# Optimization experiments

Measured on AMD Instinct MI355X. Metric: run time of the kernel, lower is better.

Reference implementation:

```python
import jax, jax.numpy as jnp
import numpy as np

C_IMG = 16
GRID = 128
NV = 100000
NE = 1600000
CH = (32, 64, 64)
SCALE = 0.1
STEPS = 1
SLOPE = 0.3  # LeakyReLU default in module


def setup_inputs() -> dict:
    key = jax.random.key(0)
    ks = jax.random.split(key, 20)
    image_features = jax.random.normal(ks[0], (C_IMG, GRID, GRID, GRID), jnp.float32)
    # vertices live in voxel coordinates of the feature grid
    vertices = jax.random.uniform(ks[1], (NV, 3), jnp.float32) * (GRID - 1)
    edge_src = jax.random.randint(ks[2], (NE,), 0, NV, jnp.int32)
    edge_dst = jax.random.randint(ks[3], (NE,), 0, NV, jnp.int32)
    dims = [C_IMG + 3] + list(CH) + [3]  # +3 normalized positions
    inp = {"image_features": image_features, "vertices": vertices,
           "edge_src": edge_src, "edge_dst": edge_dst}
    ki = 4
    for i in range(len(dims) - 1):
        fan_in = dims[i]
        s = 1.0 / np.sqrt(fan_in)
        inp[f"w_self{i}"] = jax.random.normal(ks[ki], (dims[i], dims[i + 1]), jnp.float32) * s
        inp[f"w_nb{i}"] = jax.random.normal(ks[ki + 1], (dims[i], dims[i + 1]), jnp.float32) * s
        inp[f"b{i}"] = jnp.zeros((dims[i + 1],), jnp.float32)
        ki += 2
    return inp


def trilinear_sample(img, verts):
    # img: (C, W, H, D); verts: (V, 3) voxel coords -> (V, C)
    C, W, H, D = img.shape
    hi = jnp.array([W - 1, H - 1, D - 1], verts.dtype)
    p = jnp.clip(verts, 0.0, hi)
    p0 = jnp.floor(p)
    i0 = p0.astype(jnp.int32)
    i1 = jnp.minimum(i0 + 1, hi.astype(jnp.int32))
    w = p - p0
    x0, y0, z0 = i0[:, 0], i0[:, 1], i0[:, 2]
    x1, y1, z1 = i1[:, 0], i1[:, 1], i1[:, 2]
    wx, wy, wz = w[:, 0:1], w[:, 1:2], w[:, 2:3]

    def g(xi, yi, zi):
        return img[:, xi, yi, zi].T  # (V, C)

    c00 = g(x0, y0, z0) * (1 - wz) + g(x0, y0, z1) * wz
    c01 = g(x0, y1, z0) * (1 - wz) + g(x0, y1, z1) * wz
    c10 = g(x1, y0, z0) * (1 - wz) + g(x1, y0, z1) * wz
    c11 = g(x1, y1, z0) * (1 - wz) + g(x1, y1, z1) * wz
    return (c00 * (1 - wy) + c01 * wy) * (1 - wx) + (c10 * (1 - wy) + c11 * wy) * wx


def edge_conv(x, src, dst, inv_deg, w_self, w_nb, b):
    nb = jax.ops.segment_sum(x[src], dst, num_segments=x.shape[0]) * inv_deg
    return x @ w_self + nb @ w_nb + b


def reference(image_features, vertices, edge_src, edge_dst,
              w_self0, w_nb0, b0, w_self1, w_nb1, b1,
              w_self2, w_nb2, b2, w_self3, w_nb3, b3):
    nv = vertices.shape[0]
    deg = jax.ops.segment_sum(jnp.ones((edge_src.shape[0],), jnp.float32), edge_dst,
                              num_segments=nv)
    inv_deg = (1.0 / jnp.maximum(deg, 1.0))[:, None]
    grid_max = jnp.float32(max(image_features.shape[1:]))  # image_shape.max()
    layers = [(w_self0, w_nb0, b0), (w_self1, w_nb1, b1), (w_self2, w_nb2, b2)]
    for _ in range(STEPS):
        feats = trilinear_sample(image_features, vertices)
        feats = jnp.concatenate([vertices / grid_max, feats], axis=-1)
        h = feats
        for (ws, wn, b) in layers:
            h = jax.nn.leaky_relu(edge_conv(h, edge_src, edge_dst, inv_deg, ws, wn, b), SLOPE)
        deformation = edge_conv(h, edge_src, edge_dst, inv_deg, w_self3, w_nb3, b3)
        vertices = vertices + SCALE * deformation
    return vertices
```

## Files before the change

kernel.cpp:

```cpp
#include <hip/hip_runtime.h>

#define C_IMG 16
#define GRIDSZ 128
#define VOL (GRIDSZ * GRIDSZ * GRIDSZ)
#define SLOPE 0.3f
#define SCALE 0.1f
#define EPB 4096
#define HEPB 16384
#define BIN_CAP 16384

using f4_t  = __attribute__((ext_vector_type(4))) float;
using bf8_t = __attribute__((ext_vector_type(8))) short;

__device__ __forceinline__ unsigned int bf16_pack2(float a, float b) {
    unsigned int ua = __float_as_uint(a);
    ua = (ua + 0x7FFFu + ((ua >> 16) & 1u)) >> 16;
    unsigned int ub = __float_as_uint(b);
    ub = (ub + 0x7FFFu + ((ub >> 16) & 1u)) >> 16;
    return ua | (ub << 16);
}
__device__ __forceinline__ unsigned short bf16_1(float a) {
    unsigned int ua = __float_as_uint(a);
    return (unsigned short)((ua + 0x7FFFu + ((ua >> 16) & 1u)) >> 16);
}
__device__ __forceinline__ float bf_lo(unsigned int u) { return __uint_as_float(u << 16); }
__device__ __forceinline__ float bf_hi(unsigned int u) { return __uint_as_float(u & 0xFFFF0000u); }

__global__ __launch_bounds__(256) void k_hist(const int* __restrict__ edst,
                                              int* __restrict__ bucketCount, int ne) {
    __shared__ int h[256];
    const int tid = threadIdx.x;
    h[tid] = 0;
    __syncthreads();
    const int base = blockIdx.x * HEPB;
    const int n = min(HEPB, ne - base);
    for (int i = tid; i < n; i += 256)
        atomicAdd(&h[((unsigned)edst[base + i]) >> 9], 1);
    __syncthreads();
    if (h[tid]) atomicAdd(&bucketCount[tid], h[tid]);
}

__global__ __launch_bounds__(256) void k_scan256(const int* __restrict__ bucketCount,
                                                 int* __restrict__ bucketBase,
                                                 int* __restrict__ bucketCursor,
                                                 int* __restrict__ rowStart,
                                                 int np, int nv, int ne) {
    __shared__ int buf[256];
    const int tid = threadIdx.x;
    const int v = (tid < np) ? bucketCount[tid] : 0;
    buf[tid] = v;
    __syncthreads();
    #pragma unroll
    for (int off = 1; off < 256; off <<= 1) {
        int t = (tid >= off) ? buf[tid - off] : 0;
        __syncthreads();
        buf[tid] += t;
        __syncthreads();
    }
    const int excl = buf[tid] - v;
    bucketBase[tid] = excl;
    bucketCursor[tid] = excl;
    if (tid == 0) {
        bucketBase[np] = ne;
        rowStart[nv] = ne;
    }
}

__global__ __launch_bounds__(256) void k_bucket(const int* __restrict__ esrc,
                                                const int* __restrict__ edst,
                                                int* __restrict__ bucketCursor,
                                                unsigned int* __restrict__ pairs, int ne) {
    __shared__ unsigned int hist[256];
    __shared__ unsigned int pref[256];
    __shared__ unsigned int curs[256];
    __shared__ unsigned int gbase[256];
    __shared__ unsigned int stage_v[EPB];
    __shared__ unsigned char stage_b[EPB];
    const int tid = threadIdx.x;
    const int base = blockIdx.x * EPB;
    const int n = min(EPB, ne - base);
    hist[tid] = 0;
    __syncthreads();
    for (int i = tid; i < n; i += 256)
        atomicAdd(&hist[((unsigned)edst[base + i]) >> 9], 1u);
    __syncthreads();
    const unsigned int h = hist[tid];
    pref[tid] = h;
    __syncthreads();
    #pragma unroll
    for (int off = 1; off < 256; off <<= 1) {
        unsigned int t = (tid >= off) ? pref[tid - off] : 0;
        __syncthreads();
        pref[tid] += t;
        __syncthreads();
    }
    const unsigned int excl = pref[tid] - h;
    gbase[tid] = h ? (unsigned int)atomicAdd(&bucketCursor[tid], (int)h) : 0u;
    __syncthreads();
    pref[tid] = excl;
    curs[tid] = excl;
    __syncthreads();
    for (int i = tid; i < n; i += 256) {
        unsigned int d = (unsigned)edst[base + i];
        unsigned int s = (unsigned)esrc[base + i];
        unsigned int p = atomicAdd(&curs[d >> 9], 1u);
        stage_v[p] = (s << 9) | (d & 511u);
        stage_b[p] = (unsigned char)(d >> 9);
    }
    __syncthreads();
    for (int i = tid; i < n; i += 256) {
        unsigned int b = stage_b[i];
        pairs[gbase[b] + (unsigned)i - pref[b]] = stage_v[i];
    }
}

__global__ __launch_bounds__(256) void k_binsort(const unsigned int* __restrict__ pairs,
                                                 const int* __restrict__ bucketBase,
                                                 int* __restrict__ rowStart,
                                                 float* __restrict__ invdeg,
                                                 int* __restrict__ csrSrc, int nv) {
    __shared__ int deg_s[512];
    __shared__ int rs_s[512];
    __shared__ int cur_s[512];
    __shared__ int scan_s[256];
    __shared__ int outbuf[BIN_CAP];
    const int tid = threadIdx.x;
    const int b = blockIdx.x;
    const int vbase = b << 9;
    if (vbase >= nv) return;
    const int nvb = min(512, nv - vbase);
    const int gs = bucketBase[b];
    const int ge = bucketBase[b + 1];
    const int count = ge - gs;
    deg_s[tid] = 0;
    deg_s[tid + 256] = 0;
    __syncthreads();
    for (int i = tid; i < count; i += 256) {
        unsigned int p = pairs[gs + i];
        atomicAdd(&deg_s[p & 511u], 1);
    }
    __syncthreads();
    const int d0 = deg_s[2 * tid];
    const int d1 = deg_s[2 * tid + 1];
    const int ps = d0 + d1;
    scan_s[tid] = ps;
    __syncthreads();
    #pragma unroll
    for (int off = 1; off < 256; off <<= 1) {
        int t = (tid >= off) ? scan_s[tid - off] : 0;
        __syncthreads();
        scan_s[tid] += t;
        __syncthreads();
    }
    const int epair = scan_s[tid] - ps;
    rs_s[2 * tid] = epair;
    rs_s[2 * tid + 1] = epair + d0;
    cur_s[2 * tid] = epair;
    cur_s[2 * tid + 1] = epair + d0;
    #pragma unroll
    for (int u = 0; u < 2; ++u) {
        int idx = 2 * tid + u;
        if (idx < nvb) {
            rowStart[vbase + idx] = gs + rs_s[idx];
            int d = deg_s[idx];
            invdeg[vbase + idx] = 1.0f / (float)(d > 1 ? d : 1);
        }
    }
    __syncthreads();
    if (count <= BIN_CAP) {
        for (int i = tid; i < count; i += 256) {
            unsigned int p = pairs[gs + i];
            int pos = atomicAdd(&cur_s[p & 511u], 1);
            outbuf[pos] = (int)(p >> 9);
        }
        __syncthreads();
        for (int i = tid; i < count; i += 256) csrSrc[gs + i] = outbuf[i];
    } else {
        for (int i = tid; i < count; i += 256) {
            unsigned int p = pairs[gs + i];
            int pos = atomicAdd(&cur_s[p & 511u], 1);
            csrSrc[gs + pos] = (int)(p >> 9);
        }
    }
}

__global__ __launch_bounds__(256) void k_transpose(const float* __restrict__ img,
                                                   unsigned int* __restrict__ timg) {
    const int t = blockIdx.x * 256 + threadIdx.x;
    const int q  = t & 3;
    const int z4 = (t >> 2) & 31;
    const int xy = t >> 7;
    const int z0 = z4 * 4;
    const int c0 = q * 4;
    const size_t base = (size_t)xy * GRIDSZ + z0;
    float4 v0 = *(const float4*)(img + (size_t)(c0 + 0) * VOL + base);
    float4 v1 = *(const float4*)(img + (size_t)(c0 + 1) * VOL + base);
    float4 v2 = *(const float4*)(img + (size_t)(c0 + 2) * VOL + base);
    float4 v3 = *(const float4*)(img + (size_t)(c0 + 3) * VOL + base);
    #pragma unroll
    for (int j = 0; j < 4; ++j) {
        float f0 = (j == 0) ? v0.x : (j == 1) ? v0.y : (j == 2) ? v0.z : v0.w;
        float f1 = (j == 0) ? v1.x : (j == 1) ? v1.y : (j == 2) ? v1.z : v1.w;
        float f2 = (j == 0) ? v2.x : (j == 1) ? v2.y : (j == 2) ? v2.z : v2.w;
        float f3 = (j == 0) ? v3.x : (j == 1) ? v3.y : (j == 2) ? v3.z : v3.w;
        uint2 o;
        o.x = bf16_pack2(f0, f1);
        o.y = bf16_pack2(f2, f3);
        *(uint2*)(timg + (size_t)(xy * GRIDSZ + z0 + j) * 8 + q * 2) = o;
    }
}

__global__ __launch_bounds__(256) void k_sample(const unsigned int* __restrict__ timg,
                                                const float* __restrict__ verts,
                                                unsigned int* __restrict__ feats, int nv) {
    int t = blockIdx.x * 256 + threadIdx.x;
    int v = t >> 1;
    int q = t & 1;
    if (v >= nv) return;
    float px = verts[v * 3 + 0];
    float py = verts[v * 3 + 1];
    float pz = verts[v * 3 + 2];
    float cx = fminf(fmaxf(px, 0.0f), 127.0f);
    float cy = fminf(fmaxf(py, 0.0f), 127.0f);
    float cz = fminf(fmaxf(pz, 0.0f), 127.0f);
    float fx = floorf(cx), fy = floorf(cy), fz = floorf(cz);
    int x0 = (int)fx, y0 = (int)fy, z0 = (int)fz;
    int x1 = min(x0 + 1, 127), y1 = min(y0 + 1, 127), z1 = min(z0 + 1, 127);
    float wx = cx - fx, wy = cy - fy, wz = cz - fz;
    const int qo = q * 4;
    #define LD(X, Y, Z) (*(const uint4*)(timg + ((size_t)((((X) << 7) + (Y)) << 7) + (size_t)(Z)) * 8 + qo))
    uint4 f000 = LD(x0, y0, z0), f001 = LD(x0, y0, z1);
    uint4 f010 = LD(x0, y1, z0), f011 = LD(x0, y1, z1);
    uint4 f100 = LD(x1, y0, z0), f101 = LD(x1, y0, z1);
    uint4 f110 = LD(x1, y1, z0), f111 = LD(x1, y1, z1);
    #undef LD
    float r[8];
    const unsigned int* a000 = (const unsigned int*)&f000;
    const unsigned int* a001 = (const unsigned int*)&f001;
    const unsigned int* a010 = (const unsigned int*)&f010;
    const unsigned int* a011 = (const unsigned int*)&f011;
    const unsigned int* a100 = (const unsigned int*)&f100;
    const unsigned int* a101 = (const unsigned int*)&f101;
    const unsigned int* a110 = (const unsigned int*)&f110;
    const unsigned int* a111 = (const unsigned int*)&f111;
    #pragma unroll
    for (int u = 0; u < 4; ++u) {
        float c00l = bf_lo(a000[u]) * (1.f - wz) + bf_lo(a001[u]) * wz;
        float c01l = bf_lo(a010[u]) * (1.f - wz) + bf_lo(a011[u]) * wz;
        float c10l = bf_lo(a100[u]) * (1.f - wz) + bf_lo(a101[u]) * wz;
        float c11l = bf_lo(a110[u]) * (1.f - wz) + bf_lo(a111[u]) * wz;
        r[2 * u] = (c00l * (1.f - wy) + c01l * wy) * (1.f - wx) +
                   (c10l * (1.f - wy) + c11l * wy) * wx;
        float c00h = bf_hi(a000[u]) * (1.f - wz) + bf_hi(a001[u]) * wz;
        float c01h = bf_hi(a010[u]) * (1.f - wz) + bf_hi(a011[u]) * wz;
        float c10h = bf_hi(a100[u]) * (1.f - wz) + bf_hi(a101[u]) * wz;
        float c11h = bf_hi(a110[u]) * (1.f - wz) + bf_hi(a111[u]) * wz;
        r[2 * u + 1] = (c00h * (1.f - wy) + c01h * wy) * (1.f - wx) +
                       (c10h * (1.f - wy) + c11h * wy) * wx;
    }
    unsigned int* row = feats + (size_t)v * 16;
    uint4 o;
    o.x = bf16_pack2(r[0], r[1]); o.y = bf16_pack2(r[2], r[3]);
    o.z = bf16_pack2(r[4], r[5]); o.w = bf16_pack2(r[6], r[7]);
    *(uint4*)(row + q * 4) = o;
    if (q == 0) {
        uint4 o2;
        o2.x = bf16_pack2(px * (1.0f / 128.0f), py * (1.0f / 128.0f));
        o2.y = bf16_pack2(pz * (1.0f / 128.0f), 0.0f);
        o2.z = 0u; o2.w = 0u;
        *(uint4*)(row + 8) = o2;
        *(uint4*)(row + 12) = make_uint4(0u, 0u, 0u, 0u);
    }
}

template <int SU>
__global__ __launch_bounds__(256) void k_gather16(const unsigned int* __restrict__ x,
                                                  const int* __restrict__ rowStart,
                                                  const int* __restrict__ csrSrc,
                                                  const float* __restrict__ invdeg,
                                                  unsigned int* __restrict__ nb, int nv) {
    constexpr int NCH = SU / 4;
    int t = blockIdx.x * 256 + threadIdx.x;
    int v = t / NCH;
    if (v >= nv) return;
    int ch = t - v * NCH;
    int beg = rowStart[v];
    int end = rowStart[v + 1];
    float a0 = 0.f, a1 = 0.f, a2 = 0.f, a3 = 0.f, a4 = 0.f, a5 = 0.f, a6 = 0.f, a7 = 0.f;
    int j = beg;
    for (; j + 3 < end; j += 4) {
        int s0 = csrSrc[j];
        int s1 = csrSrc[j + 1];
        int s2 = csrSrc[j + 2];
        int s3 = csrSrc[j + 3];
        uint4 q0 = ((const uint4*)(x + (size_t)s0 * SU))[ch];
        uint4 q1 = ((const uint4*)(x + (size_t)s1 * SU))[ch];
        uint4 q2 = ((const uint4*)(x + (size_t)s2 * SU))[ch];
        uint4 q3 = ((const uint4*)(x + (size_t)s3 * SU))[ch];
        a0 += bf_lo(q0.x); a1 += bf_hi(q0.x);
        a2 += bf_lo(q0.y); a3 += bf_hi(q0.y);
        a4 += bf_lo(q0.z); a5 += bf_hi(q0.z);
        a6 += bf_lo(q0.w); a7 += bf_hi(q0.w);
        a0 += bf_lo(q1.x); a1 += bf_hi(q1.x);
        a2 += bf_lo(q1.y); a3 += bf_hi(q1.y);
        a4 += bf_lo(q1.z); a5 += bf_hi(q1.z);
        a6 += bf_lo(q1.w); a7 += bf_hi(q1.w);
        a0 += bf_lo(q2.x); a1 += bf_hi(q2.x);
        a2 += bf_lo(q2.y); a3 += bf_hi(q2.y);
        a4 += bf_lo(q2.z); a5 += bf_hi(q2.z);
        a6 += bf_lo(q2.w); a7 += bf_hi(q2.w);
        a0 += bf_lo(q3.x); a1 += bf_hi(q3.x);
        a2 += bf_lo(q3.y); a3 += bf_hi(q3.y);
        a4 += bf_lo(q3.z); a5 += bf_hi(q3.z);
        a6 += bf_lo(q3.w); a7 += bf_hi(q3.w);
    }
    for (; j < end; ++j) {
        int s = csrSrc[j];
        uint4 q = ((const uint4*)(x + (size_t)s * SU))[ch];
        a0 += bf_lo(q.x); a1 += bf_hi(q.x);
        a2 += bf_lo(q.y); a3 += bf_hi(q.y);
        a4 += bf_lo(q.z); a5 += bf_hi(q.z);
        a6 += bf_lo(q.w); a7 += bf_hi(q.w);
    }
    const float id = invdeg[v];
    uint4 o;
    o.x = bf16_pack2(a0 * id, a1 * id); o.y = bf16_pack2(a2 * id, a3 * id);
    o.z = bf16_pack2(a4 * id, a5 * id); o.w = bf16_pack2(a6 * id, a7 * id);
    ((uint4*)(nb + (size_t)v * SU))[ch] = o;
}

template <int KX, int COUT, bool REMAP0, int VALID_CIN, bool PREMUL>
__global__ __launch_bounds__(256) void k_layer_mfma(const unsigned int* __restrict__ x,
                                                    const unsigned int* __restrict__ nbs,
                                                    const float* __restrict__ Ws,
                                                    const float* __restrict__ Wn,
                                                    const float* __restrict__ bias,
                                                    unsigned int* __restrict__ out, int nv,
                                                    const float* __restrict__ Wn3,
                                                    unsigned int* __restrict__ zout) {
    constexpr int KTOT = 2 * KX;
    constexpr int KW = KTOT + 8;
    constexpr int NT = COUT / 16;
    constexpr int MT = 2;
    constexpr int SXU = KX / 2;
    constexpr int KS = KX / 32;
    __shared__ __align__(16) unsigned short bt[COUT * KW];
    __shared__ float wn3_s[192];

    for (int i = threadIdx.x; i < COUT * KTOT; i += 256) {
        int c = i / KTOT;
        int kk = i - c * KTOT;
        int j = (kk < KX) ? kk : kk - KX;
        const float* W = (kk < KX) ? Ws : Wn;
        float w = 0.f;
        if (j < VALID_CIN) {
            int sr = REMAP0 ? ((j < 16) ? (j + 3) : (j - 16)) : j;
            w = W[sr * COUT + c];
        }
        bt[c * KW + kk] = bf16_1(w);
    }
    if constexpr (PREMUL) {
        if (threadIdx.x < 192) wn3_s[threadIdx.x] = Wn3[threadIdx.x];
    }
    __syncthreads();

    const int lane = threadIdx.x & 63;
    const int wid = threadIdx.x >> 6;
    const int v0 = blockIdx.x * (4 * MT * 16) + wid * (MT * 16);
    const int row = lane & 15;
    const int kg = lane >> 4;

    f4_t acc[MT][NT] = {};

    #pragma unroll
    for (int ks = 0; ks < 2 * KS; ++ks) {
        const unsigned int* src = (ks < KS) ? x : nbs;
        const int kbase = (ks < KS) ? ks * 32 : (ks - KS) * 32;
        bf8_t afrag[MT];
        #pragma unroll
        for (int mt = 0; mt < MT; ++mt) {
            int v = v0 + mt * 16 + row;
            v = min(v, nv - 1);
            afrag[mt] = *(const bf8_t*)(src + (size_t)v * SXU + ((kbase + kg * 8) >> 1));
        }
        #pragma unroll
        for (int nt = 0; nt < NT; ++nt) {
            bf8_t bfrag = *(const bf8_t*)(bt + (nt * 16 + row) * KW + ks * 32 + kg * 8);
            #pragma unroll
            for (int mt = 0; mt < MT; ++mt)
                acc[mt][nt] = __builtin_amdgcn_mfma_f32_16x16x32_bf16(afrag[mt], bfrag,
                                                                      acc[mt][nt], 0, 0, 0);
        }
    }

    unsigned short* po = (unsigned short*)out;
    float bq[NT];
    #pragma unroll
    for (int nt = 0; nt < NT; ++nt) bq[nt] = bias[nt * 16 + row];
    #pragma unroll
    for (int mt = 0; mt < MT; ++mt) {
        #pragma unroll
        for (int r = 0; r < 4; ++r) {
            const int v = v0 + mt * 16 + kg * 4 + r;
            float tv[NT];
            #pragma unroll
            for (int nt = 0; nt < NT; ++nt) {
                float t = acc[mt][nt][r] + bq[nt];
                t = (t >= 0.f) ? t : SLOPE * t;
                tv[nt] = t;
                if (v < nv) po[(size_t)v * COUT + nt * 16 + row] = bf16_1(t);
            }
            if constexpr (PREMUL) {
                float z0 = 0.f, z1 = 0.f, z2 = 0.f;
                #pragma unroll
                for (int nt = 0; nt < NT; ++nt) {
                    const float* wr = wn3_s + (nt * 16 + row) * 3;
                    z0 += tv[nt] * wr[0];
                    z1 += tv[nt] * wr[1];
                    z2 += tv[nt] * wr[2];
                }
                #pragma unroll
                for (int m = 1; m < 16; m <<= 1) {
                    z0 += __shfl_xor(z0, m);
                    z1 += __shfl_xor(z1, m);
                    z2 += __shfl_xor(z2, m);
                }
                if (row == 0 && v < nv) {
                    uint2 o;
                    o.x = bf16_pack2(z0, z1);
                    o.y = bf16_pack2(z2, 0.f);
                    *(uint2*)(zout + (size_t)v * 2) = o;
                }
            }
        }
    }
}

__global__ __launch_bounds__(256) void k_final(const unsigned int* __restrict__ h,
                                               const unsigned int* __restrict__ z,
                                               const int* __restrict__ rowStart,
                                               const int* __restrict__ csrSrc,
                                               const float* __restrict__ invdeg,
                                               const float* __restrict__ ws,
                                               const float* __restrict__ b,
                                               const float* __restrict__ verts,
                                               float* __restrict__ out, int nv) {
    __shared__ float w_s[64 * 3];
    if (threadIdx.x < 64 * 3) w_s[threadIdx.x] = ws[threadIdx.x];
    __syncthreads();
    int v = blockIdx.x * 256 + threadIdx.x;
    if (v >= nv) return;
    float n0 = 0.f, n1 = 0.f, n2 = 0.f;
    {
        int beg = rowStart[v];
        int end = rowStart[v + 1];
        int j = beg;
        for (; j + 3 < end; j += 4) {
            int s0 = csrSrc[j];
            int s1 = csrSrc[j + 1];
            int s2 = csrSrc[j + 2];
            int s3 = csrSrc[j + 3];
            uint2 q0 = *(const uint2*)(z + (size_t)s0 * 2);
            uint2 q1 = *(const uint2*)(z + (size_t)s1 * 2);
            uint2 q2 = *(const uint2*)(z + (size_t)s2 * 2);
            uint2 q3 = *(const uint2*)(z + (size_t)s3 * 2);
            n0 += bf_lo(q0.x); n1 += bf_hi(q0.x); n2 += bf_lo(q0.y);
            n0 += bf_lo(q1.x); n1 += bf_hi(q1.x); n2 += bf_lo(q1.y);
            n0 += bf_lo(q2.x); n1 += bf_hi(q2.x); n2 += bf_lo(q2.y);
            n0 += bf_lo(q3.x); n1 += bf_hi(q3.x); n2 += bf_lo(q3.y);
        }
        for (; j < end; ++j) {
            int s = csrSrc[j];
            uint2 q = *(const uint2*)(z + (size_t)s * 2);
            n0 += bf_lo(q.x); n1 += bf_hi(q.x); n2 += bf_lo(q.y);
        }
    }
    const uint4* hr = (const uint4*)(h + (size_t)v * 32);
    float a0 = b[0], a1 = b[1], a2 = b[2];
    #pragma unroll
    for (int q = 0; q < 8; ++q) {
        uint4 hv = hr[q];
        float f[8] = {bf_lo(hv.x), bf_hi(hv.x), bf_lo(hv.y), bf_hi(hv.y),
                      bf_lo(hv.z), bf_hi(hv.z), bf_lo(hv.w), bf_hi(hv.w)};
        #pragma unroll
        for (int i = 0; i < 8; ++i) {
            int k = q * 8 + i;
            a0 += f[i] * w_s[k * 3 + 0];
            a1 += f[i] * w_s[k * 3 + 1];
            a2 += f[i] * w_s[k * 3 + 2];
        }
    }
    float id = invdeg[v];
    a0 += n0 * id; a1 += n1 * id; a2 += n2 * id;
    out[(size_t)v * 3 + 0] = verts[(size_t)v * 3 + 0] + SCALE * a0;
    out[(size_t)v * 3 + 1] = verts[(size_t)v * 3 + 1] + SCALE * a1;
    out[(size_t)v * 3 + 2] = verts[(size_t)v * 3 + 2] + SCALE * a2;
}

extern "C" void kernel_launch(void* const* d_in, const int* in_sizes, int n_in,
                              void* d_out, int out_size, void* d_ws, size_t ws_size,
                              hipStream_t stream) {
    const float* img   = (const float*)d_in[0];
    const float* verts = (const float*)d_in[1];
    const int*   esrc  = (const int*)d_in[2];
    const int*   edst  = (const int*)d_in[3];
    const float* ws0 = (const float*)d_in[4];
    const float* wn0 = (const float*)d_in[5];
    const float* b0  = (const float*)d_in[6];
    const float* ws1 = (const float*)d_in[7];
    const float* wn1 = (const float*)d_in[8];
    const float* b1  = (const float*)d_in[9];
    const float* ws2 = (const float*)d_in[10];
    const float* wn2 = (const float*)d_in[11];
    const float* b2  = (const float*)d_in[12];
    const float* ws3 = (const float*)d_in[13];
    const float* wn3 = (const float*)d_in[14];
    const float* b3  = (const float*)d_in[15];

    const int nv = in_sizes[1] / 3;
    const int ne = in_sizes[2];

    char* base = (char*)d_ws;
    size_t off = 0;
    auto alloc = [&](size_t bytes) -> void* {
        off = (off + 255) & ~(size_t)255;
        void* p = base + off;
        off += bytes;
        return p;
    };
    float* invdeg   = (float*)alloc((size_t)nv * 4);
    int*   rowStart = (int*)alloc((size_t)(nv + 1) * 4);
    int*   bucketCount  = (int*)alloc(256 * 4);
    int*   bucketBase   = (int*)alloc(257 * 4);
    int*   bucketCursor = (int*)alloc(256 * 4);
    int*   csrSrc   = (int*)alloc((size_t)ne * 4);
    unsigned int* A   = (unsigned int*)alloc((size_t)nv * 32 * 4);
    unsigned int* B   = (unsigned int*)alloc((size_t)nv * 32 * 4);
    unsigned int* NBu = (unsigned int*)alloc((size_t)nv * 32 * 4);
    unsigned int* Z   = (unsigned int*)alloc((size_t)nv * 2 * 4);
    unsigned int* timg = (unsigned int*)alloc((size_t)VOL * 16 * 2);
    unsigned int* pairs = (unsigned int*)NBu;

    auto blocks = [](long long n) { return (int)((n + 255) / 256); };
    const int nbuckets = (nv + 511) >> 9;
    const int lb = (nv + 127) / 128;

    k_transpose<<<(GRIDSZ * GRIDSZ * 32 * 4) / 256, 256, 0, stream>>>(img, timg);

    hipMemsetAsync(bucketCount, 0, 256 * 4, stream);
    k_hist<<<(ne + HEPB - 1) / HEPB, 256, 0, stream>>>(edst, bucketCount, ne);
    k_scan256<<<1, 256, 0, stream>>>(bucketCount, bucketBase, bucketCursor, rowStart, nbuckets, nv, ne);
    k_bucket<<<(ne + EPB - 1) / EPB, 256, 0, stream>>>(esrc, edst, bucketCursor, pairs, ne);
    k_binsort<<<nbuckets, 256, 0, stream>>>(pairs, bucketBase, rowStart, invdeg, csrSrc, nv);

    k_sample<<<blocks((long long)nv * 2), 256, 0, stream>>>(timg, verts, A, nv);

    k_gather16<16><<<blocks((long long)nv * 4), 256, 0, stream>>>(A, rowStart, csrSrc, invdeg, NBu, nv);
    k_layer_mfma<32, 32, true, 19, false><<<lb, 256, 0, stream>>>(
        A, NBu, ws0, wn0, b0, B, nv, nullptr, nullptr);

    k_gather16<16><<<blocks((long long)nv * 4), 256, 0, stream>>>(B, rowStart, csrSrc, invdeg, NBu, nv);
    k_layer_mfma<32, 64, false, 32, false><<<lb, 256, 0, stream>>>(
        B, NBu, ws1, wn1, b1, A, nv, nullptr, nullptr);

    k_gather16<32><<<blocks((long long)nv * 8), 256, 0, stream>>>(A, rowStart, csrSrc, invdeg, NBu, nv);
    k_layer_mfma<64, 64, false, 64, true><<<lb, 256, 0, stream>>>(
        A, NBu, ws2, wn2, b2, B, nv, wn3, Z);

    k_final<<<blocks(nv), 256, 0, stream>>>(
        B, Z, rowStart, csrSrc, invdeg, ws3, b3, verts, (float*)d_out, nv);
}
```

Before: 459.6 us.

## Fuse neighbor gather into MFMA layer kernels and merge preprocessing launches

Each layer's neighbor aggregation now runs inside the MFMA layer kernel, writing the averaged neighbor features into shared memory instead of a global NB buffer. This removes the global write and re-read of the NB buffer and three kernel launches. The image transpose and edge histogram are merged into one launch, and the separate scan kernel is removed: k_bucket and k_binsort each recompute the bucket prefix redundantly per block. The cost is lower gather parallelism per vertex block, since 256 threads share 128 vertices with a serialized loop. Shared memory use per block also rises, which may reduce occupancy.

After: 454.3 us. Within noise of the previous version (-1.1%).

```diff
diff --git a/kernel.cpp b/kernel.cpp
--- a/kernel.cpp
+++ b/kernel.cpp
@@ -7,6 +7,7 @@
 #define SCALE 0.1f
 #define EPB 4096
 #define HEPB 16384
+#define TBLOCKS 8192
 #define BIN_CAP 16384
 
 using f4_t  = __attribute__((ext_vector_type(4))) float;
@@ -26,61 +27,77 @@
 __device__ __forceinline__ float bf_lo(unsigned int u) { return __uint_as_float(u << 16); }
 __device__ __forceinline__ float bf_hi(unsigned int u) { return __uint_as_float(u & 0xFFFF0000u); }
 
-__global__ __launch_bounds__(256) void k_hist(const int* __restrict__ edst,
-                                              int* __restrict__ bucketCount, int ne) {
+__global__ __launch_bounds__(256) void k_pre(const float* __restrict__ img,
+                                             unsigned int* __restrict__ timg,
+                                             const int* __restrict__ edst,
+                                             int* __restrict__ bucketCount, int ne) {
     __shared__ int h[256];
     const int tid = threadIdx.x;
-    h[tid] = 0;
-    __syncthreads();
-    const int base = blockIdx.x * HEPB;
-    const int n = min(HEPB, ne - base);
-    for (int i = tid; i < n; i += 256)
-        atomicAdd(&h[((unsigned)edst[base + i]) >> 9], 1);
-    __syncthreads();
-    if (h[tid]) atomicAdd(&bucketCount[tid], h[tid]);
-}
-
-__global__ __launch_bounds__(256) void k_scan256(const int* __restrict__ bucketCount,
-                                                 int* __restrict__ bucketBase,
-                                                 int* __restrict__ bucketCursor,
-                                                 int* __restrict__ rowStart,
-                                                 int np, int nv, int ne) {
-    __shared__ int buf[256];
-    const int tid = threadIdx.x;
-    const int v = (tid < np) ? bucketCount[tid] : 0;
-    buf[tid] = v;
-    __syncthreads();
-    #pragma unroll
-    for (int off = 1; off < 256; off <<= 1) {
-        int t = (tid >= off) ? buf[tid - off] : 0;
-        __syncthreads();
-        buf[tid] += t;
-        __syncthreads();
-    }
-    const int excl = buf[tid] - v;
-    bucketBase[tid] = excl;
-    bucketCursor[tid] = excl;
-    if (tid == 0) {
-        bucketBase[np] = ne;
-        rowStart[nv] = ne;
+    if (blockIdx.x < TBLOCKS) {
+        const int t = blockIdx.x * 256 + tid;
+        const int q  = t & 3;
+        const int z4 = (t >> 2) & 31;
+        const int xy = t >> 7;
+        const int z0 = z4 * 4;
+        const int c0 = q * 4;
+        const size_t base = (size_t)xy * GRIDSZ + z0;
+        float4 v0 = *(const float4*)(img + (size_t)(c0 + 0) * VOL + base);
+        float4 v1 = *(const float4*)(img + (size_t)(c0 + 1) * VOL + base);
+        float4 v2 = *(const float4*)(img + (size_t)(c0 + 2) * VOL + base);
+        float4 v3 = *(const float4*)(img + (size_t)(c0 + 3) * VOL + base);
+        #pragma unroll
+        for (int j = 0; j < 4; ++j) {
+            float f0 = (j == 0) ? v0.x : (j == 1) ? v0.y : (j == 2) ? v0.z : v0.w;
+            float f1 = (j == 0) ? v1.x : (j == 1) ? v1.y : (j == 2) ? v1.z : v1.w;
+            float f2 = (j == 0) ? v2.x : (j == 1) ? v2.y : (j == 2) ? v2.z : v2.w;
+            float f3 = (j == 0) ? v3.x : (j == 1) ? v3.y : (j == 2) ? v3.z : v3.w;
+            uint2 o;
+            o.x = bf16_pack2(f0, f1);
+            o.y = bf16_pack2(f2, f3);
+            *(uint2*)(timg + (size_t)(xy * GRIDSZ + z0 + j) * 8 + q * 2) = o;
+        }
+    } else {
+        h[tid] = 0;
+        __syncthreads();
+        const int base = (blockIdx.x - TBLOCKS) * HEPB;
+        const int n = min(HEPB, ne - base);
+        for (int i = tid; i < n; i += 256)
+            atomicAdd(&h[((unsigned)edst[base + i]) >> 9], 1);
+        __syncthreads();
+        if (h[tid]) atomicAdd(&bucketCount[tid], h[tid]);
     }
 }
 
 __global__ __launch_bounds__(256) void k_bucket(const int* __restrict__ esrc,
                                                 const int* __restrict__ edst,
+                                                const int* __restrict__ bucketCount,
                                                 int* __restrict__ bucketCursor,
-                                                unsigned int* __restrict__ pairs, int ne) {
+                                                unsigned int* __restrict__ pairs,
+                                                int* __restrict__ rowStart,
+                                                int ne, int nv) {
     __shared__ unsigned int hist[256];
     __shared__ unsigned int pref[256];
     __shared__ unsigned int curs[256];
     __shared__ unsigned int gbase[256];
+    __shared__ int bb[256];
     __shared__ unsigned int stage_v[EPB];
     __shared__ unsigned char stage_b[EPB];
     const int tid = threadIdx.x;
     const int base = blockIdx.x * EPB;
     const int n = min(EPB, ne - base);
+    if (blockIdx.x == 0 && tid == 0) rowStart[nv] = ne;
+    const int c = bucketCount[tid];
+    bb[tid] = c;
     hist[tid] = 0;
     __syncthreads();
+    #pragma unroll
+    for (int off = 1; off < 256; off <<= 1) {
+        int t = (tid >= off) ? bb[tid - off] : 0;
+        __syncthreads();
+        bb[tid] += t;
+        __syncthreads();
+    }
+    const int baseb = bb[tid] - c;
     for (int i = tid; i < n; i += 256)
         atomicAdd(&hist[((unsigned)edst[base + i]) >> 9], 1u);
     __syncthreads();
@@ -95,7 +112,7 @@
         __syncthreads();
     }
     const unsigned int excl = pref[tid] - h;
-    gbase[tid] = h ? (unsigned int)atomicAdd(&bucketCursor[tid], (int)h) : 0u;
+    gbase[tid] = h ? (unsigned int)(baseb + atomicAdd(&bucketCursor[tid], (int)h)) : 0u;
     __syncthreads();
     pref[tid] = excl;
     curs[tid] = excl;
@@ -115,7 +132,7 @@
 }
 
 __global__ __launch_bounds__(256) void k_binsort(const unsigned int* __restrict__ pairs,
-                                                 const int* __restrict__ bucketBase,
+                                                 const int* __restrict__ bucketCount,
                                                  int* __restrict__ rowStart,
                                                  float* __restrict__ invdeg,
                                                  int* __restrict__ csrSrc, int nv) {
@@ -123,18 +140,29 @@
     __shared__ int rs_s[512];
     __shared__ int cur_s[512];
     __shared__ int scan_s[256];
+    __shared__ int bb[256];
     __shared__ int outbuf[BIN_CAP];
     const int tid = threadIdx.x;
     const int b = blockIdx.x;
     const int vbase = b << 9;
     if (vbase >= nv) return;
     const int nvb = min(512, nv - vbase);
-    const int gs = bucketBase[b];
-    const int ge = bucketBase[b + 1];
-    const int count = ge - gs;
+    const int c = bucketCount[tid];
+    bb[tid] = c;
     deg_s[tid] = 0;
     deg_s[tid + 256] = 0;
     __syncthreads();
+    #pragma unroll
+    for (int off = 1; off < 256; off <<= 1) {
+        int t = (tid >= off) ? bb[tid - off] : 0;
+        __syncthreads();
+        bb[tid] += t;
+        __syncthreads();
+    }
+    const int cntb = bucketCount[b];
+    const int ge = bb[b];
+    const int gs = ge - cntb;
+    const int count = cntb;
     for (int i = tid; i < count; i += 256) {
         unsigned int p = pairs[gs + i];
         atomicAdd(&deg_s[p & 511u], 1);
@@ -181,32 +209,6 @@
             int pos = atomicAdd(&cur_s[p & 511u], 1);
             csrSrc[gs + pos] = (int)(p >> 9);
         }
-    }
-}
-
-__global__ __launch_bounds__(256) void k_transpose(const float* __restrict__ img,
-                                                   unsigned int* __restrict__ timg) {
-    const int t = blockIdx.x * 256 + threadIdx.x;
-    const int q  = t & 3;
-    const int z4 = (t >> 2) & 31;
-    const int xy = t >> 7;
-    const int z0 = z4 * 4;
-    const int c0 = q * 4;
-    const size_t base = (size_t)xy * GRIDSZ + z0;
-    float4 v0 = *(const float4*)(img + (size_t)(c0 + 0) * VOL + base);
-    float4 v1 = *(const float4*)(img + (size_t)(c0 + 1) * VOL + base);
-    float4 v2 = *(const float4*)(img + (size_t)(c0 + 2) * VOL + base);
-    float4 v3 = *(const float4*)(img + (size_t)(c0 + 3) * VOL + base);
-    #pragma unroll
-    for (int j = 0; j < 4; ++j) {
-        float f0 = (j == 0) ? v0.x : (j == 1) ? v0.y : (j == 2) ? v0.z : v0.w;
-        float f1 = (j == 0) ? v1.x : (j == 1) ? v1.y : (j == 2) ? v1.z : v1.w;
-        float f2 = (j == 0) ? v2.x : (j == 1) ? v2.y : (j == 2) ? v2.z : v2.w;
-        float f3 = (j == 0) ? v3.x : (j == 1) ? v3.y : (j == 2) ? v3.z : v3.w;
-        uint2 o;
-        o.x = bf16_pack2(f0, f1);
-        o.y = bf16_pack2(f2, f3);
-        *(uint2*)(timg + (size_t)(xy * GRIDSZ + z0 + j) * 8 + q * 2) = o;
     }
 }
 
@@ -273,78 +275,28 @@
     }
 }
 
-template <int SU>
-__global__ __launch_bounds__(256) void k_gather16(const unsigned int* __restrict__ x,
-                                                  const int* __restrict__ rowStart,
-                                                  const int* __restrict__ csrSrc,
-                                                  const float* __restrict__ invdeg,
-                                                  unsigned int* __restrict__ nb, int nv) {
-    constexpr int NCH = SU / 4;
-    int t = blockIdx.x * 256 + threadIdx.x;
-    int v = t / NCH;
-    if (v >= nv) return;
-    int ch = t - v * NCH;
-    int beg = rowStart[v];
-    int end = rowStart[v + 1];
-    float a0 = 0.f, a1 = 0.f, a2 = 0.f, a3 = 0.f, a4 = 0.f, a5 = 0.f, a6 = 0.f, a7 = 0.f;
-    int j = beg;
-    for (; j + 3 < end; j += 4) {
-        int s0 = csrSrc[j];
-        int s1 = csrSrc[j + 1];
-        int s2 = csrSrc[j + 2];
-        int s3 = csrSrc[j + 3];
-        uint4 q0 = ((const uint4*)(x + (size_t)s0 * SU))[ch];
-        uint4 q1 = ((const uint4*)(x + (size_t)s1 * SU))[ch];
-        uint4 q2 = ((const uint4*)(x + (size_t)s2 * SU))[ch];
-        uint4 q3 = ((const uint4*)(x + (size_t)s3 * SU))[ch];
-        a0 += bf_lo(q0.x); a1 += bf_hi(q0.x);
-        a2 += bf_lo(q0.y); a3 += bf_hi(q0.y);
-        a4 += bf_lo(q0.z); a5 += bf_hi(q0.z);
-        a6 += bf_lo(q0.w); a7 += bf_hi(q0.w);
-        a0 += bf_lo(q1.x); a1 += bf_hi(q1.x);
-        a2 += bf_lo(q1.y); a3 += bf_hi(q1.y);
-        a4 += bf_lo(q1.z); a5 += bf_hi(q1.z);
-        a6 += bf_lo(q1.w); a7 += bf_hi(q1.w);
-        a0 += bf_lo(q2.x); a1 += bf_hi(q2.x);
-        a2 += bf_lo(q2.y); a3 += bf_hi(q2.y);
-        a4 += bf_lo(q2.z); a5 += bf_hi(q2.z);
-        a6 += bf_lo(q2.w); a7 += bf_hi(q2.w);
-        a0 += bf_lo(q3.x); a1 += bf_hi(q3.x);
-        a2 += bf_lo(q3.y); a3 += bf_hi(q3.y);
-        a4 += bf_lo(q3.z); a5 += bf_hi(q3.z);
-        a6 += bf_lo(q3.w); a7 += bf_hi(q3.w);
-    }
-    for (; j < end; ++j) {
-        int s = csrSrc[j];
-        uint4 q = ((const uint4*)(x + (size_t)s * SU))[ch];
-        a0 += bf_lo(q.x); a1 += bf_hi(q.x);
-        a2 += bf_lo(q.y); a3 += bf_hi(q.y);
-        a4 += bf_lo(q.z); a5 += bf_hi(q.z);
-        a6 += bf_lo(q.w); a7 += bf_hi(q.w);
-    }
-    const float id = invdeg[v];
-    uint4 o;
-    o.x = bf16_pack2(a0 * id, a1 * id); o.y = bf16_pack2(a2 * id, a3 * id);
-    o.z = bf16_pack2(a4 * id, a5 * id); o.w = bf16_pack2(a6 * id, a7 * id);
-    ((uint4*)(nb + (size_t)v * SU))[ch] = o;
-}
-
 template <int KX, int COUT, bool REMAP0, int VALID_CIN, bool PREMUL>
-__global__ __launch_bounds__(256) void k_layer_mfma(const unsigned int* __restrict__ x,
-                                                    const unsigned int* __restrict__ nbs,
-                                                    const float* __restrict__ Ws,
-                                                    const float* __restrict__ Wn,
-                                                    const float* __restrict__ bias,
-                                                    unsigned int* __restrict__ out, int nv,
-                                                    const float* __restrict__ Wn3,
-                                                    unsigned int* __restrict__ zout) {
+__global__ __launch_bounds__(256) void k_layer_fused(const unsigned int* __restrict__ x,
+                                                     const int* __restrict__ rowStart,
+                                                     const int* __restrict__ csrSrc,
+                                                     const float* __restrict__ invdeg,
+                                                     const float* __restrict__ Ws,
+                                                     const float* __restrict__ Wn,
+                                                     const float* __restrict__ bias,
+                                                     unsigned int* __restrict__ out, int nv,
+                                                     const float* __restrict__ Wn3,
+                                                     unsigned int* __restrict__ zout) {
     constexpr int KTOT = 2 * KX;
     constexpr int KW = KTOT + 8;
     constexpr int NT = COUT / 16;
     constexpr int MT = 2;
     constexpr int SXU = KX / 2;
     constexpr int KS = KX / 32;
+    constexpr int VPB = 128;
+    constexpr int NCH = KX / 8;
+    constexpr int NBW = KX + 8;
     __shared__ __align__(16) unsigned short bt[COUT * KW];
+    __shared__ __align__(16) unsigned short nb_s[VPB * NBW];
     __shared__ float wn3_s[192];
 
     for (int i = threadIdx.x; i < COUT * KTOT; i += 256) {
@@ -362,11 +314,67 @@
     if constexpr (PREMUL) {
         if (threadIdx.x < 192) wn3_s[threadIdx.x] = Wn3[threadIdx.x];
     }
+
+    const int vb0 = blockIdx.x * VPB;
+    for (int task = threadIdx.x; task < VPB * NCH; task += 256) {
+        const int vloc = task / NCH;
+        const int ch = task - vloc * NCH;
+        const int v = vb0 + vloc;
+        unsigned short* dst = nb_s + vloc * NBW + ch * 8;
+        if (v < nv) {
+            int beg = rowStart[v];
+            int end = rowStart[v + 1];
+            float a0 = 0.f, a1 = 0.f, a2 = 0.f, a3 = 0.f,
+                  a4 = 0.f, a5 = 0.f, a6 = 0.f, a7 = 0.f;
+            int j = beg;
+            for (; j + 3 < end; j += 4) {
+                int s0 = csrSrc[j];
+                int s1 = csrSrc[j + 1];
+                int s2 = csrSrc[j + 2];
+                int s3 = csrSrc[j + 3];
+                uint4 q0 = ((const uint4*)(x + (size_t)s0 * SXU))[ch];
+                uint4 q1 = ((const uint4*)(x + (size_t)s1 * SXU))[ch];
+                uint4 q2 = ((const uint4*)(x + (size_t)s2 * SXU))[ch];
+                uint4 q3 = ((const uint4*)(x + (size_t)s3 * SXU))[ch];
+                a0 += bf_lo(q0.x); a1 += bf_hi(q0.x);
+                a2 += bf_lo(q0.y); a3 += bf_hi(q0.y);
+                a4 += bf_lo(q0.z); a5 += bf_hi(q0.z);
+                a6 += bf_lo(q0.w); a7 += bf_hi(q0.w);
+                a0 += bf_lo(q1.x); a1 += bf_hi(q1.x);
+                a2 += bf_lo(q1.y); a3 += bf_hi(q1.y);
+                a4 += bf_lo(q1.z); a5 += bf_hi(q1.z);
+                a6 += bf_lo(q1.w); a7 += bf_hi(q1.w);
+                a0 += bf_lo(q2.x); a1 += bf_hi(q2.x);
+                a2 += bf_lo(q2.y); a3 += bf_hi(q2.y);
+                a4 += bf_lo(q2.z); a5 += bf_hi(q2.z);
+                a6 += bf_lo(q2.w); a7 += bf_hi(q2.w);
+                a0 += bf_lo(q3.x); a1 += bf_hi(q3.x);
+                a2 += bf_lo(q3.y); a3 += bf_hi(q3.y);
+                a4 += bf_lo(q3.z); a5 += bf_hi(q3.z);
+                a6 += bf_lo(q3.w); a7 += bf_hi(q3.w);
+            }
+            for (; j < end; ++j) {
+                int s = csrSrc[j];
+                uint4 q = ((const uint4*)(x + (size_t)s * SXU))[ch];
+                a0 += bf_lo(q.x); a1 += bf_hi(q.x);
+                a2 += bf_lo(q.y); a3 += bf_hi(q.y);
+                a4 += bf_lo(q.z); a5 += bf_hi(q.z);
+                a6 += bf_lo(q.w); a7 += bf_hi(q.w);
+            }
+            const float id = invdeg[v];
+            uint4 o;
+            o.x = bf16_pack2(a0 * id, a1 * id); o.y = bf16_pack2(a2 * id, a3 * id);
+            o.z = bf16_pack2(a4 * id, a5 * id); o.w = bf16_pack2(a6 * id, a7 * id);
+            *(uint4*)dst = o;
+        } else {
+            *(uint4*)dst = make_uint4(0u, 0u, 0u, 0u);
+        }
+    }
     __syncthreads();
 
     const int lane = threadIdx.x & 63;
     const int wid = threadIdx.x >> 6;
-    const int v0 = blockIdx.x * (4 * MT * 16) + wid * (MT * 16);
+    const int v0 = vb0 + wid * (MT * 16);
     const int row = lane & 15;
     const int kg = lane >> 4;
 
@@ -374,14 +382,22 @@
 
     #pragma unroll
     for (int ks = 0; ks < 2 * KS; ++ks) {
-        const unsigned int* src = (ks < KS) ? x : nbs;
-        const int kbase = (ks < KS) ? ks * 32 : (ks - KS) * 32;
         bf8_t afrag[MT];
-        #pragma unroll
-        for (int mt = 0; mt < MT; ++mt) {
-            int v = v0 + mt * 16 + row;
-            v = min(v, nv - 1);
-            afrag[mt] = *(const bf8_t*)(src + (size_t)v * SXU + ((kbase + kg * 8) >> 1));
+        if (ks < KS) {
+            const int kbase = ks * 32;
+            #pragma unroll
+            for (int mt = 0; mt < MT; ++mt) {
+                int v = v0 + mt * 16 + row;
+                v = min(v, nv - 1);
+                afrag[mt] = *(const bf8_t*)(x + (size_t)v * SXU + ((kbase + kg * 8) >> 1));
+            }
+        } else {
+            const int kbase = (ks - KS) * 32;
+            #pragma unroll
+            for (int mt = 0; mt < MT; ++mt) {
+                const int vloc = wid * (MT * 16) + mt * 16 + row;
+                afrag[mt] = *(const bf8_t*)(nb_s + vloc * NBW + kbase + kg * 8);
+            }
         }
         #pragma unroll
         for (int nt = 0; nt < NT; ++nt) {
@@ -530,42 +546,37 @@
     };
     float* invdeg   = (float*)alloc((size_t)nv * 4);
     int*   rowStart = (int*)alloc((size_t)(nv + 1) * 4);
-    int*   bucketCount  = (int*)alloc(256 * 4);
-    int*   bucketBase   = (int*)alloc(257 * 4);
-    int*   bucketCursor = (int*)alloc(256 * 4);
+    int*   bcb      = (int*)alloc(512 * 4);
+    int*   bucketCount  = bcb;
+    int*   bucketCursor = bcb + 256;
     int*   csrSrc   = (int*)alloc((size_t)ne * 4);
+    unsigned int* pairs = (unsigned int*)alloc((size_t)ne * 4);
     unsigned int* A   = (unsigned int*)alloc((size_t)nv * 32 * 4);
     unsigned int* B   = (unsigned int*)alloc((size_t)nv * 32 * 4);
-    unsigned int* NBu = (unsigned int*)alloc((size_t)nv * 32 * 4);
     unsigned int* Z   = (unsigned int*)alloc((size_t)nv * 2 * 4);
     unsigned int* timg = (unsigned int*)alloc((size_t)VOL * 16 * 2);
-    unsigned int* pairs = (unsigned int*)NBu;
 
     auto blocks = [](long long n) { return (int)((n + 255) / 256); };
     const int nbuckets = (nv + 511) >> 9;
+    const int nhb = (ne + HEPB - 1) / HEPB;
     const int lb = (nv + 127) / 128;
 
-    k_transpose<<<(GRIDSZ * GRIDSZ * 32 * 4) / 256, 256, 0, stream>>>(img, timg);
-
-    hipMemsetAsync(bucketCount, 0, 256 * 4, stream);
-    k_hist<<<(ne + HEPB - 1) / HEPB, 256, 0, stream>>>(edst, bucketCount, ne);
-    k_scan256<<<1, 256, 0, stream>>>(bucketCount, bucketBase, bucketCursor, rowStart, nbuckets, nv, ne);
-    k_bucket<<<(ne + EPB - 1) / EPB, 256, 0, stream>>>(esrc, edst, bucketCursor, pairs, ne);
-    k_binsort<<<nbuckets, 256, 0, stream>>>(pairs, bucketBase, rowStart, invdeg, csrSrc, nv);
+    hipMemsetAsync(bcb, 0, 512 * 4, stream);
+    k_pre<<<TBLOCKS + nhb, 256, 0, stream>>>(img, timg, edst, bucketCount, ne);
+    k_bucket<<<(ne + EPB - 1) / EPB, 256, 0, stream>>>(esrc, edst, bucketCount, bucketCursor,
+                                                       pairs, rowStart, ne, nv);
+    k_binsort<<<nbuckets, 256, 0, stream>>>(pairs, bucketCount, rowStart, invdeg, csrSrc, nv);
 
     k_sample<<<blocks((long long)nv * 2), 256, 0, stream>>>(timg, verts, A, nv);
 
-    k_gather16<16><<<blocks((long long)nv * 4), 256, 0, stream>>>(A, rowStart, csrSrc, invdeg, NBu, nv);
-    k_layer_mfma<32, 32, true, 19, false><<<lb, 256, 0, stream>>>(
-        A, NBu, ws0, wn0, b0, B, nv, nullptr, nullptr);
-
-    k_gather16<16><<<blocks((long long)nv * 4), 256, 0, stream>>>(B, rowStart, csrSrc, invdeg, NBu, nv);
-    k_layer_mfma<32, 64, false, 32, false><<<lb, 256, 0, stream>>>(
-        B, NBu, ws1, wn1, b1, A, nv, nullptr, nullptr);
-
-    k_gather16<32><<<blocks((long long)nv * 8), 256, 0, stream>>>(A, rowStart, csrSrc, invdeg, NBu, nv);
-    k_layer_mfma<64, 64, false, 64, true><<<lb, 256, 0, stream>>>(
-        A, NBu, ws2, wn2, b2, B, nv, wn3, Z);
+    k_layer_fused<32, 32, true, 19, false><<<lb, 256, 0, stream>>>(
+        A, rowStart, csrSrc, invdeg, ws0, wn0, b0, B, nv, nullptr, nullptr);
+
+    k_layer_fused<32, 64, false, 32, false><<<lb, 256, 0, stream>>>(
+        B, rowStart, csrSrc, invdeg, ws1, wn1, b1, A, nv, nullptr, nullptr);
+
+    k_layer_fused<64, 64, false, 64, true><<<lb, 256, 0, stream>>>(
+        A, rowStart, csrSrc, invdeg, ws2, wn2, b2, B, nv, wn3, Z);
 
     k_final<<<blocks(nv), 256, 0, stream>>>(
         B, Z, rowStart, csrSrc, invdeg, ws3, b3, verts, (float*)d_out, nv);
```
